# Performance work log

Measured on AMD Instinct MI355X. Metric: run time of the kernel, lower is better.

The kernel has to match this reference:

```python
import jax, jax.numpy as jnp
import numpy as np

N, E, B = 50000, 800000, 16
IN_DIM, ED, HD, SD, NC = 64, 8, 128, 128, 8
T_STEPS = (8 + 16) // 2  # eval mode: (t_min + t_max) // 2 = 12


def setup_inputs() -> dict:
    key = jax.random.key(0)
    ks = jax.random.split(key, 12)
    s = 0.05  # small init scale so 12 residual steps stay bounded
    return {
        "x": jax.random.normal(ks[0], (N, IN_DIM), jnp.float32),
        "edge_index": jax.random.randint(ks[1], (2, E), 0, N, jnp.int64),
        "edge_attr": jax.random.normal(ks[2], (E, ED), jnp.float32),
        "batch": jnp.sort(jax.random.randint(ks[3], (N,), 0, B, jnp.int64)),
        "enc_w": jax.random.normal(ks[4], (IN_DIM, SD), jnp.float32) * s,
        "enc_b": jnp.zeros((SD,), jnp.float32),
        "msg_w": jax.random.normal(ks[5], (SD + ED, HD), jnp.float32) * s,
        "msg_b": jnp.zeros((HD,), jnp.float32),
        "up_w1": jax.random.normal(ks[6], (SD + HD, HD), jnp.float32) * s,
        "up_b1": jnp.zeros((HD,), jnp.float32),
        "up_w2": jax.random.normal(ks[7], (HD, SD), jnp.float32) * s,
        "up_b2": jnp.zeros((SD,), jnp.float32),
    }


def reference(x, edge_index, edge_attr, batch, enc_w, enc_b, msg_w, msg_b,
              up_w1, up_b1, up_w2, up_b2):
    src, dst = edge_index[0], edge_index[1]  # x_j = x[src], aggregate at dst
    # in-degree for mean aggregation (zero-degree nodes get 0, clamp avoids /0)
    deg = jax.ops.segment_sum(jnp.ones((E,), x.dtype), dst, num_segments=N)
    deg = jnp.clip(deg, 1.0)[:, None]

    # Encoder: Linear + ReLU
    state = jax.nn.relu(x @ enc_w + enc_b)  # [N, SD]

    for _ in range(T_STEPS):
        # message: relu(W_msg @ [h_j || e_ji])
        m = jax.nn.relu(jnp.concatenate([state[src], edge_attr], axis=-1) @ msg_w + msg_b)  # [E, HD]
        agg = jax.ops.segment_sum(m, dst, num_segments=N) / deg  # scatter-mean [N, HD]
        # update MLP on [h_i || m_bar_i]
        h = jax.nn.relu(jnp.concatenate([state, agg], axis=-1) @ up_w1 + up_b1)
        delta = h @ up_w2 + up_b2
        state = state + delta  # eval: no stochastic mask, no noise

    # Readout: per-graph mean over class channels
    class_ch = state[:, -NC:]  # [N, NC]
    cnt = jax.ops.segment_sum(jnp.ones((N,), x.dtype), batch, num_segments=B)
    logits = jax.ops.segment_sum(class_ch, batch, num_segments=B) / jnp.clip(cnt, 1.0)[:, None]
    return logits
```

## Files before the change

kernel.cpp:

```cpp
#include <hip/hip_runtime.h>
#include <hip/hip_bf16.h>

#define NN 50000
#define NE 800000
#define NB 16
#define T_STEPS 12
#define SCAN_B 196
#define EAW_BLOCKS 2048

typedef __attribute__((ext_vector_type(8))) short short8;
typedef __attribute__((ext_vector_type(4))) float f32x4;
typedef __attribute__((ext_vector_type(2))) float f32x2;
typedef unsigned short u16;
typedef unsigned int u32;

__device__ __forceinline__ float bf2f(u32 u) {
    union { u32 i; float f; } v; v.i = u << 16; return v.f;
}
__device__ __forceinline__ u16 f2bf(float f) {
    union { float f; u32 i; } v; v.f = f;
    u32 r = v.i + 0x7fffu + ((v.i >> 16) & 1u);
    return (u16)(r >> 16);
}
__device__ __forceinline__ f32x4 mfma16(short8 a, short8 b, f32x4 c) {
    return __builtin_amdgcn_mfma_f32_16x16x32_bf16(a, b, c, 0, 0, 0);
}

__device__ __forceinline__ u32 pk2_fp8(float o0, float o1) {
#if __has_builtin(__builtin_amdgcn_cvt_pk_fp8_f32)
    return (u32)__builtin_amdgcn_cvt_pk_fp8_f32(o0, o1, 0, false);
#else
    u32 a = 0;
    asm("v_cvt_pk_fp8_f32 %0, %1, %2" : "+v"(a) : "v"(o0), "v"(o1));
    return a;
#endif
}
__device__ __forceinline__ u32 pk4_fp8(float o0, float o1, float o2, float o3) {
    return (pk2_fp8(o0, o1) & 0xffffu) | (pk2_fp8(o2, o3) << 16);
}
__device__ __forceinline__ unsigned char f2fp8b(float v) {
    return (unsigned char)(pk2_fp8(v, 0.f) & 0xffu);
}

__device__ __forceinline__ void fp8x4f(u32 w, float& f0, float& f1, float& f2, float& f3) {
#if __has_builtin(__builtin_amdgcn_cvt_pk_f32_fp8)
    f32x2 r0 = __builtin_amdgcn_cvt_pk_f32_fp8((int)w, false);
    f32x2 r1 = __builtin_amdgcn_cvt_pk_f32_fp8((int)w, true);
    f0 = r0[0]; f1 = r0[1]; f2 = r1[0]; f3 = r1[1];
#else
    f32x2 r0, r1;
    u32 hi = w >> 16;
    asm("v_cvt_pk_f32_fp8 %0, %1" : "=v"(r0) : "v"(w));
    asm("v_cvt_pk_f32_fp8 %0, %1" : "=v"(r1) : "v"(hi));
    f0 = r0[0]; f1 = r0[1]; f2 = r1[0]; f3 = r1[1];
#endif
}

#define W1OFF 0
#define W2OFF 32768
#define WSOFF 49152
#define ENCOFF 65536
#define PACKN 73728


__global__ void k_hist(const int* __restrict__ dst, int* __restrict__ hist) {
    int e = blockIdx.x * 256 + threadIdx.x;
    if (e < NE) atomicAdd(&hist[dst[e]], 1);
}

__global__ void k_scanA(const int* __restrict__ hist, int* __restrict__ excl,
                        int* __restrict__ bsum) {
    __shared__ int sh[256];
    int t = threadIdx.x, b = blockIdx.x;
    int idx = b * 256 + t;
    int v = (idx < NN) ? hist[idx] : 0;
    sh[t] = v;
    __syncthreads();
    for (int off = 1; off < 256; off <<= 1) {
        int add = (t >= off) ? sh[t - off] : 0;
        __syncthreads();
        sh[t] += add;
        __syncthreads();
    }
    if (idx < NN) excl[idx] = sh[t] - v;
    if (t == 255) bsum[b] = sh[255];
}

__global__ void k_scanB(int* __restrict__ bsum) {
    __shared__ int sh[256];
    int t = threadIdx.x;
    int v = (t < SCAN_B) ? bsum[t] : 0;
    sh[t] = v;
    __syncthreads();
    for (int off = 1; off < 256; off <<= 1) {
        int add = (t >= off) ? sh[t - off] : 0;
        __syncthreads();
        sh[t] += add;
        __syncthreads();
    }
    if (t < SCAN_B) bsum[t] = sh[t] - v;
}

__global__ void k_scanC(const int* __restrict__ excl, const int* __restrict__ bsum,
                        int* __restrict__ rowptr, int* __restrict__ cursor) {
    int idx = blockIdx.x * 256 + threadIdx.x;
    if (idx < NN) {
        int r = excl[idx] + bsum[blockIdx.x];
        rowptr[idx] = r;
        cursor[idx] = r;
    }
    if (idx == 0) rowptr[NN] = NE;
}

__global__ void k_scatter(const int* __restrict__ src, const int* __restrict__ dst,
                          const float* __restrict__ eattr, int* __restrict__ cursor,
                          int* __restrict__ ssrc, u16* __restrict__ ea8) {
    int e = blockIdx.x * 256 + threadIdx.x;
    if (e >= NE) return;
    int d = dst[e];
    int pos = atomicAdd(&cursor[d], 1);
    ssrc[pos] = src[e];
    const float* ap = eattr + (size_t)e * 8;
    uint4 w;
    w.x = (u32)f2bf(ap[0]) | ((u32)f2bf(ap[1]) << 16);
    w.y = (u32)f2bf(ap[2]) | ((u32)f2bf(ap[3]) << 16);
    w.z = (u32)f2bf(ap[4]) | ((u32)f2bf(ap[5]) << 16);
    w.w = (u32)f2bf(ap[6]) | ((u32)f2bf(ap[7]) << 16);
    *(uint4*)(ea8 + (size_t)pos * 8) = w;
}

__global__ __launch_bounds__(256) void k_eaw(
    const u16* __restrict__ ea8, const float* __restrict__ msg_w,
    unsigned char* __restrict__ eaw) {
    const int tid = threadIdx.x;
    const int hex = tid & 15;
    const int esub = tid >> 4;
    float w[8][8];
#pragma unroll
    for (int k = 0; k < 8; ++k) {
        float4 v0 = *(const float4*)(msg_w + (size_t)(128 + k) * 128 + hex * 8);
        float4 v1 = *(const float4*)(msg_w + (size_t)(128 + k) * 128 + hex * 8 + 4);
        w[k][0] = v0.x; w[k][1] = v0.y; w[k][2] = v0.z; w[k][3] = v0.w;
        w[k][4] = v1.x; w[k][5] = v1.y; w[k][6] = v1.z; w[k][7] = v1.w;
    }
    int p = blockIdx.x * 16 + esub;
    if (p >= NE) return;
    uint4 ev = *(const uint4*)(ea8 + (size_t)p * 8);
    while (true) {
        int pn = p + EAW_BLOCKS * 16;
        bool more = pn < NE;
        uint4 evn;
        if (more) evn = *(const uint4*)(ea8 + (size_t)pn * 8);
        float ef[8];
        ef[0] = bf2f(ev.x & 0xffffu); ef[1] = bf2f(ev.x >> 16);
        ef[2] = bf2f(ev.y & 0xffffu); ef[3] = bf2f(ev.y >> 16);
        ef[4] = bf2f(ev.z & 0xffffu); ef[5] = bf2f(ev.z >> 16);
        ef[6] = bf2f(ev.w & 0xffffu); ef[7] = bf2f(ev.w >> 16);
        float o[8];
#pragma unroll
        for (int c = 0; c < 8; ++c) o[c] = ef[0] * w[0][c];
#pragma unroll
        for (int k = 1; k < 8; ++k)
#pragma unroll
            for (int c = 0; c < 8; ++c) o[c] += ef[k] * w[k][c];
        uint2 q;
        q.x = pk4_fp8(o[0], o[1], o[2], o[3]);
        q.y = pk4_fp8(o[4], o[5], o[6], o[7]);
        *(uint2*)(eaw + (size_t)p * 128 + hex * 8) = q;
        if (!more) break;
        p = pn;
        ev = evn;
    }
}

__global__ void k_pack(const float* __restrict__ up_w1, const float* __restrict__ up_w2,
                       const float* __restrict__ msg_w, const float* __restrict__ enc_w,
                       u16* __restrict__ packed) {
    int idx = blockIdx.x * 256 + threadIdx.x;
    if (idx >= PACKN) return;
    const float* srcp; int local;
    if (idx < W2OFF)        { srcp = up_w1; local = idx; }
    else if (idx < WSOFF)   { srcp = up_w2; local = idx - W2OFF; }
    else if (idx < ENCOFF)  { srcp = msg_w; local = idx - WSOFF; }
    else                    { srcp = enc_w; local = idx - ENCOFF; }
    int j = local & 7;
    int l = (local >> 3) & 63;
    int ntks = local >> 9;
    int nt = ntks & 7;
    int ks = ntks >> 3;
    int krow = ks * 32 + (l >> 4) * 8 + j;
    int col = nt * 16 + (l & 15);
    packed[idx] = f2bf(srcp[krow * 128 + col]);
}


__global__ __launch_bounds__(256) void k_encode(
    const float* __restrict__ x, const float* __restrict__ enc_b,
    const float* __restrict__ msg_b, const u16* __restrict__ packed,
    u16* __restrict__ state_h, unsigned char* __restrict__ swf8) {
    __shared__ u16 stage[4][2048];
    const int wv = threadIdx.x >> 6, l = threadIdx.x & 63;
    const int lr = l & 15, kb = l >> 4;
    const int rb = blockIdx.x * 64 + wv * 16;
    const int row = rb + lr;
    const int rowc = row < NN ? row : NN - 1;

    f32x4 acc[8] = {};
#pragma unroll
    for (int ks = 0; ks < 2; ++ks) {
        const float* ap = x + (size_t)rowc * 64 + ks * 32 + kb * 8;
        float4 a0 = *(const float4*)ap;
        float4 a1 = *(const float4*)(ap + 4);
        short8 a;
        a[0] = (short)f2bf(a0.x); a[1] = (short)f2bf(a0.y);
        a[2] = (short)f2bf(a0.z); a[3] = (short)f2bf(a0.w);
        a[4] = (short)f2bf(a1.x); a[5] = (short)f2bf(a1.y);
        a[6] = (short)f2bf(a1.z); a[7] = (short)f2bf(a1.w);
        const u16* bp = packed + ENCOFF + (size_t)(ks * 512 + l) * 8;
#pragma unroll
        for (int nt = 0; nt < 8; ++nt) {
            short8 b = *(const short8*)(bp + nt * 512);
            acc[nt] = mfma16(a, b, acc[nt]);
        }
    }
#pragma unroll
    for (int nt = 0; nt < 8; ++nt) {
        int col = nt * 16 + lr;
        float bias = enc_b[col];
#pragma unroll
        for (int j = 0; j < 4; ++j) {
            int rl = kb * 4 + j;
            int r = rb + rl;
            float v = acc[nt][j] + bias;
            v = v > 0.f ? v : 0.f;
            u16 h = f2bf(v);
            if (r < NN) state_h[(size_t)r * 128 + col] = h;
            int byte = (rl * 256 + col * 2) ^ ((rl & 7) << 4);
            *(u16*)((char*)stage[wv] + byte) = h;
        }
    }
    f32x4 acc3[8] = {};
#pragma unroll
    for (int ks = 0; ks < 4; ++ks) {
        int byte = (lr * 256 + ks * 64 + kb * 16) ^ ((lr & 7) << 4);
        short8 a = *(const short8*)((char*)stage[wv] + byte);
        const u16* bp = packed + WSOFF + (size_t)(ks * 512 + l) * 8;
#pragma unroll
        for (int nt = 0; nt < 8; ++nt) {
            short8 b = *(const short8*)(bp + nt * 512);
            acc3[nt] = mfma16(a, b, acc3[nt]);
        }
    }
#pragma unroll
    for (int nt = 0; nt < 8; ++nt) {
        int col = nt * 16 + lr;
        float bias = msg_b[col];
#pragma unroll
        for (int j = 0; j < 4; ++j) {
            int r = rb + kb * 4 + j;
            if (r < NN) swf8[(size_t)r * 128 + col] = f2fp8b(acc3[nt][j] + bias);
        }
    }
}


__global__ __launch_bounds__(256) void k_edge(
    const int* __restrict__ rowptr, const int* __restrict__ ssrc,
    const unsigned char* __restrict__ eaw, const unsigned char* __restrict__ swf8,
    u16* __restrict__ aggb) {
    __shared__ float red[4][2][4][129];
    const int wv = threadIdx.x >> 6, l = threadIdx.x & 63;
    const int half = l >> 5;
    const int slot = (l >> 3) & 3;
    const int g = l & 7;
    const int n = blockIdx.x * 8 + wv * 2 + half;
    if (n >= NN) return;
    const int e0 = rowptr[n], e1 = rowptr[n + 1];
    float acc[16];
#pragma unroll
    for (int c = 0; c < 16; ++c) acc[c] = 0.f;

    int i = e0 + slot;
    uint4 qc = {0, 0, 0, 0}, sac = {0, 0, 0, 0};
    if (i < e1) {
        int sc = ssrc[i];
        qc = *(const uint4*)(eaw + (size_t)i * 128 + g * 16);
        sac = *(const uint4*)(swf8 + (size_t)sc * 128 + g * 16);
    }
    int inext = i + 4;
    int snext = (inext < e1) ? ssrc[inext] : 0;
    while (i < e1) {
        int i2 = inext + 4;
        int s2 = (i2 < e1) ? ssrc[i2] : 0;
        uint4 qn = {0, 0, 0, 0}, san = {0, 0, 0, 0};
        if (inext < e1) {
            qn = *(const uint4*)(eaw + (size_t)inext * 128 + g * 16);
            san = *(const uint4*)(swf8 + (size_t)snext * 128 + g * 16);
        }
        float ef[16], sw[16];
        fp8x4f(qc.x, ef[0], ef[1], ef[2], ef[3]);
        fp8x4f(qc.y, ef[4], ef[5], ef[6], ef[7]);
        fp8x4f(qc.z, ef[8], ef[9], ef[10], ef[11]);
        fp8x4f(qc.w, ef[12], ef[13], ef[14], ef[15]);
        fp8x4f(sac.x, sw[0], sw[1], sw[2], sw[3]);
        fp8x4f(sac.y, sw[4], sw[5], sw[6], sw[7]);
        fp8x4f(sac.z, sw[8], sw[9], sw[10], sw[11]);
        fp8x4f(sac.w, sw[12], sw[13], sw[14], sw[15]);
#pragma unroll
        for (int c = 0; c < 16; ++c) {
            float m = sw[c] + ef[c];
            acc[c] += m > 0.f ? m : 0.f;
        }
        qc = qn; sac = san;
        i = inext;
        inext = i2;
        snext = s2;
    }
    float* rp = &red[wv][half][slot][g * 16];
#pragma unroll
    for (int c = 0; c < 16; c += 4) {
        f32x4 v = {acc[c], acc[c + 1], acc[c + 2], acc[c + 3]};
        *(f32x4*)(rp + c) = v;
    }
    const int lo = l & 31;
    const int ch = lo * 4;
    f32x4 sum = *(const f32x4*)&red[wv][half][0][ch];
#pragma unroll
    for (int sl = 1; sl < 4; ++sl) {
        f32x4 v = *(const f32x4*)&red[wv][half][sl][ch];
        sum[0] += v[0]; sum[1] += v[1]; sum[2] += v[2]; sum[3] += v[3];
    }
    int dg = e1 - e0;
    float inv = 1.f / (float)(dg > 0 ? dg : 1);
    uint2 outw;
    outw.x = (u32)f2bf(sum[0] * inv) | ((u32)f2bf(sum[1] * inv) << 16);
    outw.y = (u32)f2bf(sum[2] * inv) | ((u32)f2bf(sum[3] * inv) << 16);
    *(uint2*)(aggb + (size_t)n * 128 + ch) = outw;
}


__global__ __launch_bounds__(256) void k_update(
    const float* __restrict__ up_b1, const float* __restrict__ up_b2,
    const float* __restrict__ msg_b, const u16* __restrict__ packed,
    const u16* __restrict__ aggb, u16* __restrict__ state_h,
    unsigned char* __restrict__ swf8) {
    __shared__ u16 stage[4][2][2048];
    const int wv = threadIdx.x >> 6, l = threadIdx.x & 63;
    const int lr = l & 15, kb = l >> 4;
    const int rbase = blockIdx.x * 128 + wv * 32;

    f32x4 acc[2][8] = {};
#pragma unroll
    for (int ks = 0; ks < 8; ++ks) {
        short8 a[2];
#pragma unroll
        for (int rt = 0; rt < 2; ++rt) {
            int row = rbase + rt * 16 + lr;
            int rowc = row < NN ? row : NN - 1;
            const u16* abase = (ks < 4)
                ? (state_h + (size_t)rowc * 128 + ks * 32 + kb * 8)
                : (aggb + (size_t)rowc * 128 + (ks - 4) * 32 + kb * 8);
            a[rt] = *(const short8*)abase;
        }
        const u16* bp = packed + W1OFF + (size_t)(ks * 512 + l) * 8;
#pragma unroll
        for (int nt = 0; nt < 8; ++nt) {
            short8 b = *(const short8*)(bp + nt * 512);
            acc[0][nt] = mfma16(a[0], b, acc[0][nt]);
            acc[1][nt] = mfma16(a[1], b, acc[1][nt]);
        }
    }
#pragma unroll
    for (int nt = 0; nt < 8; ++nt) {
        int col = nt * 16 + lr;
        float b1v = up_b1[col];
#pragma unroll
        for (int rt = 0; rt < 2; ++rt) {
#pragma unroll
            for (int j = 0; j < 4; ++j) {
                int rl = kb * 4 + j;
                float v = acc[rt][nt][j] + b1v;
                v = v > 0.f ? v : 0.f;
                int byte = (rl * 256 + col * 2) ^ ((rl & 7) << 4);
                *(u16*)((char*)stage[wv][rt] + byte) = f2bf(v);
            }
        }
    }
    f32x4 acc2[2][8] = {};
#pragma unroll
    for (int ks = 0; ks < 4; ++ks) {
        int byte = (lr * 256 + ks * 64 + kb * 16) ^ ((lr & 7) << 4);
        short8 a[2];
        a[0] = *(const short8*)((char*)stage[wv][0] + byte);
        a[1] = *(const short8*)((char*)stage[wv][1] + byte);
        const u16* bp = packed + W2OFF + (size_t)(ks * 512 + l) * 8;
#pragma unroll
        for (int nt = 0; nt < 8; ++nt) {
            short8 b = *(const short8*)(bp + nt * 512);
            acc2[0][nt] = mfma16(a[0], b, acc2[0][nt]);
            acc2[1][nt] = mfma16(a[1], b, acc2[1][nt]);
        }
    }
#pragma unroll
    for (int rt = 0; rt < 2; ++rt) {
#pragma unroll
        for (int nt = 0; nt < 8; ++nt) {
            int col = nt * 16 + lr;
            float b2v = up_b2[col];
#pragma unroll
            for (int j = 0; j < 4; ++j) {
                int rl = kb * 4 + j;
                int r = rbase + rt * 16 + rl;
                int rc = r < NN ? r : NN - 1;
                float sold = bf2f((u32)state_h[(size_t)rc * 128 + col]);
                float snew = sold + acc2[rt][nt][j] + b2v;
                u16 hb = f2bf(snew);
                if (r < NN) state_h[(size_t)r * 128 + col] = hb;
                int byte = (rl * 256 + col * 2) ^ ((rl & 7) << 4);
                *(u16*)((char*)stage[wv][rt] + byte) = hb;
            }
        }
    }
    f32x4 acc3[2][8] = {};
#pragma unroll
    for (int ks = 0; ks < 4; ++ks) {
        int byte = (lr * 256 + ks * 64 + kb * 16) ^ ((lr & 7) << 4);
        short8 a[2];
        a[0] = *(const short8*)((char*)stage[wv][0] + byte);
        a[1] = *(const short8*)((char*)stage[wv][1] + byte);
        const u16* bp = packed + WSOFF + (size_t)(ks * 512 + l) * 8;
#pragma unroll
        for (int nt = 0; nt < 8; ++nt) {
            short8 b = *(const short8*)(bp + nt * 512);
            acc3[0][nt] = mfma16(a[0], b, acc3[0][nt]);
            acc3[1][nt] = mfma16(a[1], b, acc3[1][nt]);
        }
    }
#pragma unroll
    for (int rt = 0; rt < 2; ++rt) {
#pragma unroll
        for (int nt = 0; nt < 8; ++nt) {
            int col = nt * 16 + lr;
            float bias = msg_b[col];
#pragma unroll
            for (int j = 0; j < 4; ++j) {
                int r = rbase + rt * 16 + kb * 4 + j;
                if (r < NN) swf8[(size_t)r * 128 + col] = f2fp8b(acc3[rt][nt][j] + bias);
            }
        }
    }
}


__global__ void k_logits(const u16* __restrict__ state_h, const int* __restrict__ batch,
                         float* __restrict__ out) {
    __shared__ float red[256];
    int b = blockIdx.x, t = threadIdx.x;
    int ch = t & 7, sub = t >> 3;
    int lo = 0, hi = NN;
    while (lo < hi) { int m = (lo + hi) >> 1; if (batch[m] < b) lo = m + 1; else hi = m; }
    int s0 = lo;
    lo = 0; hi = NN;
    while (lo < hi) { int m = (lo + hi) >> 1; if (batch[m] < b + 1) lo = m + 1; else hi = m; }
    int s1 = lo;
    float acc = 0.f;
    for (int n = s0 + sub; n < s1; n += 32)
        acc += bf2f((u32)state_h[(size_t)n * 128 + 120 + ch]);
    red[t] = acc;
    __syncthreads();
    for (int off = 16; off >= 1; off >>= 1) {
        if (sub < off) red[t] += red[t + off * 8];
        __syncthreads();
    }
    if (sub == 0) {
        int c = s1 - s0;
        float cnt = (float)(c > 0 ? c : 1);
        out[b * 8 + ch] = red[ch] / cnt;
    }
}


extern "C" void kernel_launch(void* const* d_in, const int* in_sizes, int n_in,
                              void* d_out, int out_size, void* d_ws, size_t ws_size,
                              hipStream_t stream) {
    (void)in_sizes; (void)n_in;
    const float* x      = (const float*)d_in[0];
    const int*   eidx   = (const int*)d_in[1];
    const float* eattr  = (const float*)d_in[2];
    const int*   batch  = (const int*)d_in[3];
    const float* enc_w  = (const float*)d_in[4];
    const float* enc_b  = (const float*)d_in[5];
    const float* msg_w  = (const float*)d_in[6];
    const float* msg_b  = (const float*)d_in[7];
    const float* up_w1  = (const float*)d_in[8];
    const float* up_b1  = (const float*)d_in[9];
    const float* up_w2  = (const float*)d_in[10];
    const float* up_b2  = (const float*)d_in[11];
    const int* esrc = eidx;
    const int* edst = eidx + NE;

    char* p = (char*)d_ws;
    size_t off = 0;
    auto carve = [&](size_t bytes) -> char* {
        char* r = p + off;
        off += (bytes + 255) & ~(size_t)255;
        return r;
    };
    u16* state_h   = (u16*)carve((size_t)NN * 128 * 2);
    u16* aggb      = (u16*)carve((size_t)NN * 128 * 2);
    unsigned char* swf8 = (unsigned char*)carve((size_t)NN * 128);
    int* ssrc      = (int*)carve((size_t)NE * 4);
    u16* ea8       = (u16*)carve((size_t)NE * 8 * 2);
    unsigned char* eaw = (unsigned char*)carve((size_t)NE * 128);
    int* rowptr    = (int*)carve((size_t)(NN + 1) * 4);
    int* cursor    = (int*)carve((size_t)NN * 4);
    int* hist      = (int*)carve((size_t)NN * 4);
    int* sexcl     = (int*)carve((size_t)NN * 4);
    int* bsum      = (int*)carve((size_t)256 * 4);
    u16* packed    = (u16*)carve((size_t)PACKN * 2);
    if (off > ws_size) {
        hipMemsetAsync(d_out, 0xFF, (size_t)out_size * 4, stream);
        return;
    }

    hipMemsetAsync(hist, 0, (size_t)NN * 4, stream);
    k_hist<<<(NE + 255) / 256, 256, 0, stream>>>(edst, hist);
    k_scanA<<<SCAN_B, 256, 0, stream>>>(hist, sexcl, bsum);
    k_scanB<<<1, 256, 0, stream>>>(bsum);
    k_scanC<<<SCAN_B, 256, 0, stream>>>(sexcl, bsum, rowptr, cursor);
    k_scatter<<<(NE + 255) / 256, 256, 0, stream>>>(esrc, edst, eattr, cursor, ssrc, ea8);
    k_eaw<<<EAW_BLOCKS, 256, 0, stream>>>(ea8, msg_w, eaw);
    k_pack<<<(PACKN + 255) / 256, 256, 0, stream>>>(up_w1, up_w2, msg_w, enc_w, packed);
    k_encode<<<(NN + 63) / 64, 256, 0, stream>>>(x, enc_b, msg_b, packed, state_h, swf8);
    for (int t = 0; t < T_STEPS; ++t) {
        k_edge<<<(NN + 7) / 8, 256, 0, stream>>>(rowptr, ssrc, eaw, swf8, aggb);
        k_update<<<(NN + 127) / 128, 256, 0, stream>>>(up_b1, up_b2, msg_b, packed, aggb,
                                                       state_h, swf8);
    }
    k_logits<<<NB, 256, 0, stream>>>(state_h, batch, (float*)d_out);
}
```

Measured before the change: 1.031 ms.

## Assign one wavefront per node in edge kernel with shuffle reduction; shrink update blocks

The edge aggregation kernel now gives each destination node a full 64-lane wavefront, with 8 edge slots instead of 4, and reduces the partial sums across slots with cross-lane shuffles instead of a shared-memory staging buffer. This doubles the edge-level parallelism per node and removes the LDS round trip. The trade-off is that low-degree nodes leave more lanes idle and the grid has twice as many blocks. The update kernel is also shrunk to 128-thread blocks covering 64 rows, giving more, smaller blocks for better occupancy and load balance.

```diff
diff --git a/kernel.cpp b/kernel.cpp
--- a/kernel.cpp
+++ b/kernel.cpp
@@ -268,12 +268,10 @@
     const int* __restrict__ rowptr, const int* __restrict__ ssrc,
     const unsigned char* __restrict__ eaw, const unsigned char* __restrict__ swf8,
     u16* __restrict__ aggb) {
-    __shared__ float red[4][2][4][129];
     const int wv = threadIdx.x >> 6, l = threadIdx.x & 63;
-    const int half = l >> 5;
-    const int slot = (l >> 3) & 3;
+    const int slot = l >> 3;
     const int g = l & 7;
-    const int n = blockIdx.x * 8 + wv * 2 + half;
+    const int n = blockIdx.x * 4 + wv;
     if (n >= NN) return;
     const int e0 = rowptr[n], e1 = rowptr[n + 1];
     float acc[16];
@@ -287,10 +285,10 @@
         qc = *(const uint4*)(eaw + (size_t)i * 128 + g * 16);
         sac = *(const uint4*)(swf8 + (size_t)sc * 128 + g * 16);
     }
-    int inext = i + 4;
+    int inext = i + 8;
     int snext = (inext < e1) ? ssrc[inext] : 0;
     while (i < e1) {
-        int i2 = inext + 4;
+        int i2 = inext + 8;
         int s2 = (i2 < e1) ? ssrc[i2] : 0;
         uint4 qn = {0, 0, 0, 0}, san = {0, 0, 0, 0};
         if (inext < e1) {
@@ -316,38 +314,39 @@
         inext = i2;
         snext = s2;
     }
-    float* rp = &red[wv][half][slot][g * 16];
-#pragma unroll
-    for (int c = 0; c < 16; c += 4) {
-        f32x4 v = {acc[c], acc[c + 1], acc[c + 2], acc[c + 3]};
-        *(f32x4*)(rp + c) = v;
-    }
-    const int lo = l & 31;
-    const int ch = lo * 4;
-    f32x4 sum = *(const f32x4*)&red[wv][half][0][ch];
-#pragma unroll
-    for (int sl = 1; sl < 4; ++sl) {
-        f32x4 v = *(const f32x4*)&red[wv][half][sl][ch];
-        sum[0] += v[0]; sum[1] += v[1]; sum[2] += v[2]; sum[3] += v[3];
-    }
-    int dg = e1 - e0;
-    float inv = 1.f / (float)(dg > 0 ? dg : 1);
-    uint2 outw;
-    outw.x = (u32)f2bf(sum[0] * inv) | ((u32)f2bf(sum[1] * inv) << 16);
-    outw.y = (u32)f2bf(sum[2] * inv) | ((u32)f2bf(sum[3] * inv) << 16);
-    *(uint2*)(aggb + (size_t)n * 128 + ch) = outw;
-}
-
-
-__global__ __launch_bounds__(256) void k_update(
+#pragma unroll
+    for (int c = 0; c < 16; ++c) acc[c] += __shfl_xor(acc[c], 8);
+#pragma unroll
+    for (int c = 0; c < 16; ++c) acc[c] += __shfl_xor(acc[c], 16);
+#pragma unroll
+    for (int c = 0; c < 16; ++c) acc[c] += __shfl_xor(acc[c], 32);
+    if (slot == 0) {
+        int dg = e1 - e0;
+        float inv = 1.f / (float)(dg > 0 ? dg : 1);
+        uint4 w0, w1;
+        w0.x = (u32)f2bf(acc[0] * inv)  | ((u32)f2bf(acc[1] * inv) << 16);
+        w0.y = (u32)f2bf(acc[2] * inv)  | ((u32)f2bf(acc[3] * inv) << 16);
+        w0.z = (u32)f2bf(acc[4] * inv)  | ((u32)f2bf(acc[5] * inv) << 16);
+        w0.w = (u32)f2bf(acc[6] * inv)  | ((u32)f2bf(acc[7] * inv) << 16);
+        w1.x = (u32)f2bf(acc[8] * inv)  | ((u32)f2bf(acc[9] * inv) << 16);
+        w1.y = (u32)f2bf(acc[10] * inv) | ((u32)f2bf(acc[11] * inv) << 16);
+        w1.z = (u32)f2bf(acc[12] * inv) | ((u32)f2bf(acc[13] * inv) << 16);
+        w1.w = (u32)f2bf(acc[14] * inv) | ((u32)f2bf(acc[15] * inv) << 16);
+        *(uint4*)(aggb + (size_t)n * 128 + g * 16) = w0;
+        *(uint4*)(aggb + (size_t)n * 128 + g * 16 + 8) = w1;
+    }
+}
+
+
+__global__ __launch_bounds__(128) void k_update(
     const float* __restrict__ up_b1, const float* __restrict__ up_b2,
     const float* __restrict__ msg_b, const u16* __restrict__ packed,
     const u16* __restrict__ aggb, u16* __restrict__ state_h,
     unsigned char* __restrict__ swf8) {
-    __shared__ u16 stage[4][2][2048];
+    __shared__ u16 stage[2][2][2048];
     const int wv = threadIdx.x >> 6, l = threadIdx.x & 63;
     const int lr = l & 15, kb = l >> 4;
-    const int rbase = blockIdx.x * 128 + wv * 32;
+    const int rbase = blockIdx.x * 64 + wv * 32;
 
     f32x4 acc[2][8] = {};
 #pragma unroll
@@ -533,9 +532,9 @@
     k_pack<<<(PACKN + 255) / 256, 256, 0, stream>>>(up_w1, up_w2, msg_w, enc_w, packed);
     k_encode<<<(NN + 63) / 64, 256, 0, stream>>>(x, enc_b, msg_b, packed, state_h, swf8);
     for (int t = 0; t < T_STEPS; ++t) {
-        k_edge<<<(NN + 7) / 8, 256, 0, stream>>>(rowptr, ssrc, eaw, swf8, aggb);
-        k_update<<<(NN + 127) / 128, 256, 0, stream>>>(up_b1, up_b2, msg_b, packed, aggb,
-                                                       state_h, swf8);
+        k_edge<<<(NN + 3) / 4, 256, 0, stream>>>(rowptr, ssrc, eaw, swf8, aggb);
+        k_update<<<(NN + 63) / 64, 128, 0, stream>>>(up_b1, up_b2, msg_b, packed, aggb,
+                                                     state_h, swf8);
     }
     k_logits<<<NB, 256, 0, stream>>>(state_h, batch, (float*)d_out);
 }
```

Measured after the change: 1.037 ms (median of 2 runs). Within noise of the previous version (+0.6%).
